# Kernel optimization log

Hardware: AMD Instinct MI355X
Metric: run time of the kernel (lower is better)

Reference implementation:

```python
import jax, jax.numpy as jnp
import numpy as np

B, S, D = 4, 2048, 1024
E, F, K = 8, 4096, 2  # num_experts, mlp_dim, experts_per_token


def setup_inputs() -> dict:
    key = jax.random.key(0)
    ks = jax.random.split(key, 5)
    scale_d = 1.0 / np.sqrt(D)
    scale_f = 1.0 / np.sqrt(F)
    return {
        "x": jax.random.normal(ks[0], (B, S, D), dtype=jnp.float32),
        "gate_w": jax.random.normal(ks[1], (D, E), dtype=jnp.float32) * scale_d,
        "wi0": jax.random.normal(ks[2], (E, D, F), dtype=jnp.float32) * scale_d,
        "wi1": jax.random.normal(ks[3], (E, D, F), dtype=jnp.float32) * scale_d,
        "wo": jax.random.normal(ks[4], (E, F, D), dtype=jnp.float32) * scale_f,
    }


def reference(x, gate_w, wi0, wi1, wo):
    # Gating: [B,S,E] logits -> top-k values/indices -> softmax over the k selected
    gate_logits = jnp.einsum("bsd,de->bse", x, gate_w)
    topk_w, topk_idx = jax.lax.top_k(gate_logits, K)  # [B,S,K]
    topk_w = jax.nn.softmax(topk_w, axis=-1)

    num_experts = wi0.shape[0]
    out = jnp.zeros_like(x)
    # Faithful to the naive MoE loop: every expert MLP runs over all tokens,
    # output masked/weighted by the token's gate weight for that expert.
    for e in range(num_experts):
        w_e = jnp.sum((topk_idx == e) * topk_w, axis=-1)  # [B,S]
        h = jax.nn.silu(jnp.einsum("bsd,df->bsf", x, wi0[e])) * jnp.einsum(
            "bsd,df->bsf", x, wi1[e]
        )  # gated SiLU MLP intermediate [B,S,F]
        out = out + w_e[..., None] * jnp.einsum("bsf,fd->bsd", h, wo[e])
    return out
```

## Files before the change

kernel.cpp:

```cpp
#include <hip/hip_runtime.h>
#include <math.h>

#define TOKENS 8192
#define DDIM 1024
#define FDIM 4096
#define NEXP 8
#define CAP 8192
#define BM 128
#define BN 128
#define BK 32

typedef __bf16 bf16x8 __attribute__((ext_vector_type(8)));
typedef float f32x4 __attribute__((ext_vector_type(4)));

__device__ __forceinline__ unsigned short f2bf(float f) {
  union { float f; unsigned int u; } v; v.f = f;
  unsigned int u = v.u;
  return (unsigned short)((u + 0x7FFFu + ((u >> 16) & 1u)) >> 16);
}
__device__ __forceinline__ float bf2f(unsigned short h) {
  union { unsigned int u; float f; } v; v.u = ((unsigned int)h) << 16;
  return v.f;
}

__device__ __forceinline__ void load_lds16(const void* g, void* l) {
  __builtin_amdgcn_global_load_lds(
      (const __attribute__((address_space(1))) void*)g,
      (__attribute__((address_space(3))) void*)l, 16, 0, 0);
}


__global__ void k_convert_x(const float* __restrict__ x, unsigned short* __restrict__ xb) {
  int i = (blockIdx.x * 256 + threadIdx.x) * 4;
  float4 v = *(const float4*)(x + i);
  ushort4 o;
  o.x = f2bf(v.x); o.y = f2bf(v.y); o.z = f2bf(v.z); o.w = f2bf(v.w);
  *(ushort4*)(xb + i) = o;
}

__global__ void k_tconv(const float* __restrict__ in, unsigned short* __restrict__ out,
                        int R, int C) {
  __shared__ float tile[32][132];
  size_t mat = (size_t)R * C;
  const float* src = in + (size_t)blockIdx.z * mat;
  unsigned short* dst = out + (size_t)blockIdx.z * mat;
  int c0 = blockIdx.x * 128, r0 = blockIdx.y * 32;
  int t = threadIdx.x;
#pragma unroll
  for (int i = 0; i < 4; ++i) {
    int idx = i * 1024 + t * 4;
    int r = idx >> 7, c = idx & 127;
    float4 v = *(const float4*)(src + (size_t)(r0 + r) * C + (c0 + c));
    *(float4*)&tile[r][c] = v;
  }
  __syncthreads();
#pragma unroll
  for (int i = 0; i < 4; ++i) {
    int idx = i * 1024 + t * 4;
    int c = idx >> 5, r = idx & 31;
    ushort4 o;
    o.x = f2bf(tile[r + 0][c]);
    o.y = f2bf(tile[r + 1][c]);
    o.z = f2bf(tile[r + 2][c]);
    o.w = f2bf(tile[r + 3][c]);
    *(ushort4*)(dst + (size_t)(c0 + c) * R + (r0 + r)) = o;
  }
}


__global__ void k_zero(int* __restrict__ counts) {
  if (threadIdx.x < NEXP) counts[threadIdx.x] = 0;
}

__global__ void k_gate(const float* __restrict__ x, const float* __restrict__ gw,
                       int* __restrict__ counts, int* __restrict__ tok_list,
                       float* __restrict__ wgt_list, int* __restrict__ tok_slot) {
  int wave = threadIdx.x >> 6, lane = threadIdx.x & 63;
  int t = blockIdx.x * 4 + wave;
  const float* xr = x + (size_t)t * DDIM;
  float acc[NEXP];
#pragma unroll
  for (int e = 0; e < NEXP; ++e) acc[e] = 0.f;
  for (int d = lane; d < DDIM; d += 64) {
    float xv = xr[d];
    const float* g = gw + d * NEXP;
#pragma unroll
    for (int e = 0; e < NEXP; ++e) acc[e] += xv * g[e];
  }
#pragma unroll
  for (int e = 0; e < NEXP; ++e) {
#pragma unroll
    for (int off = 32; off > 0; off >>= 1) acc[e] += __shfl_down(acc[e], off, 64);
  }
  if (lane == 0) {
    int e0 = 0; float v0 = acc[0];
#pragma unroll
    for (int e = 1; e < NEXP; ++e) if (acc[e] > v0) { v0 = acc[e]; e0 = e; }
    int e1 = -1; float v1 = -3.0e38f;
#pragma unroll
    for (int e = 0; e < NEXP; ++e) if (e != e0 && acc[e] > v1) { v1 = acc[e]; e1 = e; }
    float p1 = expf(v1 - v0);
    float s = 1.0f + p1;
    float w0 = 1.0f / s, w1 = p1 / s;
    int pos0 = atomicAdd(&counts[e0], 1);
    tok_list[e0 * CAP + pos0] = t;
    wgt_list[e0 * CAP + pos0] = w0;
    tok_slot[t * 2 + 0] = e0 * CAP + pos0;
    int pos1 = atomicAdd(&counts[e1], 1);
    tok_list[e1 * CAP + pos1] = t;
    wgt_list[e1 * CAP + pos1] = w1;
    tok_slot[t * 2 + 1] = e1 * CAP + pos1;
  }
}

__global__ void k_scan(const int* __restrict__ counts, int* __restrict__ bases) {
  if (threadIdx.x == 0) {
    int s = 0;
    for (int e = 0; e < NEXP; ++e) { bases[e] = s; s += counts[e]; }
  }
}


__global__ __launch_bounds__(256, 2) void k_gemm1(
    const unsigned short* __restrict__ xb, const unsigned short* __restrict__ w0t,
    const unsigned short* __restrict__ w1t, const int* __restrict__ counts,
    const int* __restrict__ bases, const int* __restrict__ tok_list,
    unsigned short* __restrict__ H) {
  int e = blockIdx.z, mt = blockIdx.y, nt = blockIdx.x;
  int cnt = counts[e];
  int m0 = mt * BM;
  if (m0 >= cnt) return;
  int mv = min(BM, cnt - m0);
  int gbase = bases[e] + m0;

  __shared__ __align__(16) unsigned short As[BM * BK];
  __shared__ __align__(16) unsigned short B0s[BN * BK];
  __shared__ __align__(16) unsigned short B1s[BN * BK];
  __shared__ int toks[BM];

  int t = threadIdx.x;
  if (t < BM) toks[t] = tok_list[e * CAP + m0 + min(t, mv - 1)];
  __syncthreads();

  int wid = t >> 6, lane = t & 63;
  int wm = (wid >> 1) * 64, wn = (wid & 1) * 64;
  int fr = lane & 15, fq = lane >> 4;
  int csl = fq ^ ((fr >> 1) & 3);

  int row0 = t >> 2,        row1 = (t + 256) >> 2;
  int fq0 = (t & 3) ^ ((row0 >> 1) & 3);
  int fq1 = ((t + 256) & 3) ^ ((row1 >> 1) & 3);

  f32x4 acc0[4][4], acc1[4][4];
#pragma unroll
  for (int mi = 0; mi < 4; ++mi)
#pragma unroll
    for (int ni = 0; ni < 4; ++ni)
#pragma unroll
      for (int r = 0; r < 4; ++r) { acc0[mi][ni][r] = 0.f; acc1[mi][ni][r] = 0.f; }

  const unsigned short* b0p = w0t + ((size_t)e * FDIM + nt * BN) * DDIM;
  const unsigned short* b1p = w1t + ((size_t)e * FDIM + nt * BN) * DDIM;
  const size_t arow0 = (size_t)toks[row0] * DDIM;
  const size_t arow1 = (size_t)toks[row1] * DDIM;

  for (int kt = 0; kt < DDIM; kt += BK) {
    load_lds16(xb + arow0 + kt + fq0 * 8, As + t * 8);
    load_lds16(xb + arow1 + kt + fq1 * 8, As + (t + 256) * 8);
    load_lds16(b0p + (size_t)row0 * DDIM + kt + fq0 * 8, B0s + t * 8);
    load_lds16(b0p + (size_t)row1 * DDIM + kt + fq1 * 8, B0s + (t + 256) * 8);
    load_lds16(b1p + (size_t)row0 * DDIM + kt + fq0 * 8, B1s + t * 8);
    load_lds16(b1p + (size_t)row1 * DDIM + kt + fq1 * 8, B1s + (t + 256) * 8);
    __syncthreads();
    bf16x8 a[4], b0[4], b1[4];
#pragma unroll
    for (int mi = 0; mi < 4; ++mi)
      a[mi] = *(const bf16x8*)(As + (wm + mi * 16 + fr) * BK + csl * 8);
#pragma unroll
    for (int ni = 0; ni < 4; ++ni) {
      b0[ni] = *(const bf16x8*)(B0s + (wn + ni * 16 + fr) * BK + csl * 8);
      b1[ni] = *(const bf16x8*)(B1s + (wn + ni * 16 + fr) * BK + csl * 8);
    }
#pragma unroll
    for (int mi = 0; mi < 4; ++mi)
#pragma unroll
      for (int ni = 0; ni < 4; ++ni) {
        acc0[mi][ni] = __builtin_amdgcn_mfma_f32_16x16x32_bf16(a[mi], b0[ni], acc0[mi][ni], 0, 0, 0);
        acc1[mi][ni] = __builtin_amdgcn_mfma_f32_16x16x32_bf16(a[mi], b1[ni], acc1[mi][ni], 0, 0, 0);
      }
    __syncthreads();
  }

  int n0 = nt * BN + wn;
#pragma unroll
  for (int mi = 0; mi < 4; ++mi) {
    int mloc = wm + mi * 16 + fq * 4;
#pragma unroll
    for (int ni = 0; ni < 4; ++ni) {
      int col = n0 + ni * 16 + fr;
#pragma unroll
      for (int r = 0; r < 4; ++r) {
        int mrow = mloc + r;
        if (mrow < mv) {
          float g = acc0[mi][ni][r];
          float hv = (g / (1.0f + expf(-g))) * acc1[mi][ni][r];
          H[(size_t)(gbase + mrow) * FDIM + col] = f2bf(hv);
        }
      }
    }
  }
}


__global__ __launch_bounds__(256, 2) void k_gemm2(
    const unsigned short* __restrict__ H, const unsigned short* __restrict__ wot,
    const int* __restrict__ counts, const int* __restrict__ bases,
    unsigned short* __restrict__ O) {
  int e = blockIdx.z, mt = blockIdx.y, nt = blockIdx.x;
  int cnt = counts[e];
  int m0 = mt * BM;
  if (m0 >= cnt) return;
  int mv = min(BM, cnt - m0);
  int gbase = bases[e] + m0;

  __shared__ __align__(16) unsigned short As[BM * BK];
  __shared__ __align__(16) unsigned short Bs[BN * BK];

  int t = threadIdx.x;
  int wid = t >> 6, lane = t & 63;
  int wm = (wid >> 1) * 64, wn = (wid & 1) * 64;
  int fr = lane & 15, fq = lane >> 4;
  int csl = fq ^ ((fr >> 1) & 3);

  int row0 = t >> 2,        row1 = (t + 256) >> 2;
  int fq0 = (t & 3) ^ ((row0 >> 1) & 3);
  int fq1 = ((t + 256) & 3) ^ ((row1 >> 1) & 3);

  f32x4 acc[4][4];
#pragma unroll
  for (int mi = 0; mi < 4; ++mi)
#pragma unroll
    for (int ni = 0; ni < 4; ++ni)
#pragma unroll
      for (int r = 0; r < 4; ++r) acc[mi][ni][r] = 0.f;

  const unsigned short* bp = wot + ((size_t)e * DDIM + nt * BN) * FDIM;
  const size_t arow0 = (size_t)(gbase + min(row0, mv - 1)) * FDIM;
  const size_t arow1 = (size_t)(gbase + min(row1, mv - 1)) * FDIM;

  for (int kt = 0; kt < FDIM; kt += BK) {
    load_lds16(H + arow0 + kt + fq0 * 8, As + t * 8);
    load_lds16(H + arow1 + kt + fq1 * 8, As + (t + 256) * 8);
    load_lds16(bp + (size_t)row0 * FDIM + kt + fq0 * 8, Bs + t * 8);
    load_lds16(bp + (size_t)row1 * FDIM + kt + fq1 * 8, Bs + (t + 256) * 8);
    __syncthreads();
    bf16x8 a[4], b[4];
#pragma unroll
    for (int mi = 0; mi < 4; ++mi)
      a[mi] = *(const bf16x8*)(As + (wm + mi * 16 + fr) * BK + csl * 8);
#pragma unroll
    for (int ni = 0; ni < 4; ++ni)
      b[ni] = *(const bf16x8*)(Bs + (wn + ni * 16 + fr) * BK + csl * 8);
#pragma unroll
    for (int mi = 0; mi < 4; ++mi)
#pragma unroll
      for (int ni = 0; ni < 4; ++ni)
        acc[mi][ni] = __builtin_amdgcn_mfma_f32_16x16x32_bf16(a[mi], b[ni], acc[mi][ni], 0, 0, 0);
    __syncthreads();
  }

  int n0 = nt * BN + wn;
#pragma unroll
  for (int mi = 0; mi < 4; ++mi) {
    int mloc = wm + mi * 16 + fq * 4;
#pragma unroll
    for (int ni = 0; ni < 4; ++ni) {
      int col = n0 + ni * 16 + fr;
#pragma unroll
      for (int r = 0; r < 4; ++r) {
        int mrow = mloc + r;
        if (mrow < mv)
          O[(size_t)(gbase + mrow) * DDIM + col] = f2bf(acc[mi][ni][r]);
      }
    }
  }
}


__global__ void k_combine(const unsigned short* __restrict__ O, const int* __restrict__ bases,
                          const int* __restrict__ tok_slot, const float* __restrict__ wgt_list,
                          float* __restrict__ out) {
  int t = blockIdx.x;
  int s0 = tok_slot[t * 2 + 0];
  int s1 = tok_slot[t * 2 + 1];
  int g0 = bases[s0 / CAP] + (s0 & (CAP - 1));
  int g1 = bases[s1 / CAP] + (s1 & (CAP - 1));
  float w0 = wgt_list[s0], w1 = wgt_list[s1];
  int d = threadIdx.x * 4;
  ushort4 a = *(const ushort4*)(O + (size_t)g0 * DDIM + d);
  ushort4 b = *(const ushort4*)(O + (size_t)g1 * DDIM + d);
  float4 r;
  r.x = w0 * bf2f(a.x) + w1 * bf2f(b.x);
  r.y = w0 * bf2f(a.y) + w1 * bf2f(b.y);
  r.z = w0 * bf2f(a.z) + w1 * bf2f(b.z);
  r.w = w0 * bf2f(a.w) + w1 * bf2f(b.w);
  *(float4*)(out + (size_t)t * DDIM + d) = r;
}


extern "C" void kernel_launch(void* const* d_in, const int* in_sizes, int n_in,
                              void* d_out, int out_size, void* d_ws, size_t ws_size,
                              hipStream_t stream) {
  const float* x   = (const float*)d_in[0];
  const float* gw  = (const float*)d_in[1];
  const float* wi0 = (const float*)d_in[2];
  const float* wi1 = (const float*)d_in[3];
  const float* wo  = (const float*)d_in[4];
  float* out = (float*)d_out;

  char* p = (char*)d_ws;
  unsigned short* xb  = (unsigned short*)p; p += (size_t)TOKENS * DDIM * 2;
  unsigned short* w0t = (unsigned short*)p; p += (size_t)NEXP * FDIM * DDIM * 2;
  unsigned short* w1t = (unsigned short*)p; p += (size_t)NEXP * FDIM * DDIM * 2;
  unsigned short* wot = (unsigned short*)p; p += (size_t)NEXP * DDIM * FDIM * 2;
  unsigned short* H   = (unsigned short*)p; p += (size_t)2 * TOKENS * FDIM * 2;
  unsigned short* O   = (unsigned short*)p; p += (size_t)2 * TOKENS * DDIM * 2;
  int*   counts   = (int*)p; p += 256;
  int*   bases    = (int*)p; p += 256;
  int*   tok_list = (int*)p; p += (size_t)NEXP * CAP * 4;
  float* wgt_list = (float*)p; p += (size_t)NEXP * CAP * 4;
  int*   tok_slot = (int*)p; p += (size_t)TOKENS * 2 * 4;

  k_convert_x<<<(TOKENS * DDIM) / 1024, 256, 0, stream>>>(x, xb);
  k_tconv<<<dim3(FDIM / 128, DDIM / 32, NEXP), 256, 0, stream>>>(wi0, w0t, DDIM, FDIM);
  k_tconv<<<dim3(FDIM / 128, DDIM / 32, NEXP), 256, 0, stream>>>(wi1, w1t, DDIM, FDIM);
  k_tconv<<<dim3(DDIM / 128, FDIM / 32, NEXP), 256, 0, stream>>>(wo, wot, FDIM, DDIM);

  k_zero<<<1, 64, 0, stream>>>(counts);
  k_gate<<<TOKENS / 4, 256, 0, stream>>>(x, gw, counts, tok_list, wgt_list, tok_slot);
  k_scan<<<1, 64, 0, stream>>>(counts, bases);

  k_gemm1<<<dim3(FDIM / BN, CAP / BM, NEXP), 256, 0, stream>>>(xb, w0t, w1t, counts, bases, tok_list, H);
  k_gemm2<<<dim3(DDIM / BN, CAP / BM, NEXP), 256, 0, stream>>>(H, wot, counts, bases, O);

  k_combine<<<TOKENS, 256, 0, stream>>>(O, bases, tok_slot, wgt_list, out);
}
```

Before: 1.267 ms.

## Double GEMM K-tile, remap blocks for XCD locality, fuse x conversion into gating

```diff
diff --git a/kernel.cpp b/kernel.cpp
--- a/kernel.cpp
+++ b/kernel.cpp
@@ -8,7 +8,7 @@
 #define CAP 8192
 #define BM 128
 #define BN 128
-#define BK 32
+#define BK 64
 
 typedef __bf16 bf16x8 __attribute__((ext_vector_type(8)));
 typedef float f32x4 __attribute__((ext_vector_type(4)));
@@ -27,15 +27,6 @@
   __builtin_amdgcn_global_load_lds(
       (const __attribute__((address_space(1))) void*)g,
       (__attribute__((address_space(3))) void*)l, 16, 0, 0);
-}
-
-
-__global__ void k_convert_x(const float* __restrict__ x, unsigned short* __restrict__ xb) {
-  int i = (blockIdx.x * 256 + threadIdx.x) * 4;
-  float4 v = *(const float4*)(x + i);
-  ushort4 o;
-  o.x = f2bf(v.x); o.y = f2bf(v.y); o.z = f2bf(v.z); o.w = f2bf(v.w);
-  *(ushort4*)(xb + i) = o;
 }
 
 __global__ void k_tconv(const float* __restrict__ in, unsigned short* __restrict__ out,
@@ -73,16 +64,19 @@
 }
 
 __global__ void k_gate(const float* __restrict__ x, const float* __restrict__ gw,
+                       unsigned short* __restrict__ xb,
                        int* __restrict__ counts, int* __restrict__ tok_list,
                        float* __restrict__ wgt_list, int* __restrict__ tok_slot) {
   int wave = threadIdx.x >> 6, lane = threadIdx.x & 63;
   int t = blockIdx.x * 4 + wave;
   const float* xr = x + (size_t)t * DDIM;
+  unsigned short* xbr = xb + (size_t)t * DDIM;
   float acc[NEXP];
 #pragma unroll
   for (int e = 0; e < NEXP; ++e) acc[e] = 0.f;
   for (int d = lane; d < DDIM; d += 64) {
     float xv = xr[d];
+    xbr[d] = f2bf(xv);
     const float* g = gw + d * NEXP;
 #pragma unroll
     for (int e = 0; e < NEXP; ++e) acc[e] += xv * g[e];
@@ -121,12 +115,20 @@
 }
 
 
+
 __global__ __launch_bounds__(256, 2) void k_gemm1(
     const unsigned short* __restrict__ xb, const unsigned short* __restrict__ w0t,
     const unsigned short* __restrict__ w1t, const int* __restrict__ counts,
     const int* __restrict__ bases, const int* __restrict__ tok_list,
     unsigned short* __restrict__ H) {
-  int e = blockIdx.z, mt = blockIdx.y, nt = blockIdx.x;
+  int b = blockIdx.x;
+  int xcd = b & 7, j = b >> 3;
+  int i8 = j & 7, grp = j >> 3;
+  int G = grp * 8 + xcd;
+  int e = G >> 8;
+  int mt = (G >> 2) & 63;
+  int nt = ((G & 3) << 3) | i8;
+
   int cnt = counts[e];
   int m0 = mt * BM;
   if (m0 >= cnt) return;
@@ -145,11 +147,20 @@
   int wid = t >> 6, lane = t & 63;
   int wm = (wid >> 1) * 64, wn = (wid & 1) * 64;
   int fr = lane & 15, fq = lane >> 4;
-  int csl = fq ^ ((fr >> 1) & 3);
-
-  int row0 = t >> 2,        row1 = (t + 256) >> 2;
-  int fq0 = (t & 3) ^ ((row0 >> 1) & 3);
-  int fq1 = ((t + 256) & 3) ^ ((row1 >> 1) & 3);
+  int sw = fr & 7;
+  int co0 = (fq ^ sw) * 8;
+  int co1 = ((4 | fq) ^ sw) * 8;
+
+  int srow[4], soff[4];
+#pragma unroll
+  for (int r = 0; r < 4; ++r) {
+    int s = t + r * 256;
+    srow[r] = s >> 3;
+    soff[r] = ((s & 7) ^ (srow[r] & 7)) * 8;
+  }
+  size_t arow[4];
+#pragma unroll
+  for (int r = 0; r < 4; ++r) arow[r] = (size_t)toks[srow[r]] * DDIM + soff[r];
 
   f32x4 acc0[4][4], acc1[4][4];
 #pragma unroll
@@ -161,33 +172,36 @@
 
   const unsigned short* b0p = w0t + ((size_t)e * FDIM + nt * BN) * DDIM;
   const unsigned short* b1p = w1t + ((size_t)e * FDIM + nt * BN) * DDIM;
-  const size_t arow0 = (size_t)toks[row0] * DDIM;
-  const size_t arow1 = (size_t)toks[row1] * DDIM;
 
   for (int kt = 0; kt < DDIM; kt += BK) {
-    load_lds16(xb + arow0 + kt + fq0 * 8, As + t * 8);
-    load_lds16(xb + arow1 + kt + fq1 * 8, As + (t + 256) * 8);
-    load_lds16(b0p + (size_t)row0 * DDIM + kt + fq0 * 8, B0s + t * 8);
-    load_lds16(b0p + (size_t)row1 * DDIM + kt + fq1 * 8, B0s + (t + 256) * 8);
-    load_lds16(b1p + (size_t)row0 * DDIM + kt + fq0 * 8, B1s + t * 8);
-    load_lds16(b1p + (size_t)row1 * DDIM + kt + fq1 * 8, B1s + (t + 256) * 8);
+#pragma unroll
+    for (int r = 0; r < 4; ++r) {
+      int s = t + r * 256;
+      load_lds16(xb + arow[r] + kt, As + s * 8);
+      load_lds16(b0p + (size_t)srow[r] * DDIM + soff[r] + kt, B0s + s * 8);
+      load_lds16(b1p + (size_t)srow[r] * DDIM + soff[r] + kt, B1s + s * 8);
+    }
     __syncthreads();
-    bf16x8 a[4], b0[4], b1[4];
-#pragma unroll
-    for (int mi = 0; mi < 4; ++mi)
-      a[mi] = *(const bf16x8*)(As + (wm + mi * 16 + fr) * BK + csl * 8);
-#pragma unroll
-    for (int ni = 0; ni < 4; ++ni) {
-      b0[ni] = *(const bf16x8*)(B0s + (wn + ni * 16 + fr) * BK + csl * 8);
-      b1[ni] = *(const bf16x8*)(B1s + (wn + ni * 16 + fr) * BK + csl * 8);
-    }
-#pragma unroll
-    for (int mi = 0; mi < 4; ++mi)
+#pragma unroll
+    for (int kh = 0; kh < 2; ++kh) {
+      int co = kh ? co1 : co0;
+      bf16x8 a[4], b0[4], b1[4];
+#pragma unroll
+      for (int mi = 0; mi < 4; ++mi)
+        a[mi] = *(const bf16x8*)(As + (wm + mi * 16 + fr) * BK + co);
 #pragma unroll
       for (int ni = 0; ni < 4; ++ni) {
-        acc0[mi][ni] = __builtin_amdgcn_mfma_f32_16x16x32_bf16(a[mi], b0[ni], acc0[mi][ni], 0, 0, 0);
-        acc1[mi][ni] = __builtin_amdgcn_mfma_f32_16x16x32_bf16(a[mi], b1[ni], acc1[mi][ni], 0, 0, 0);
+        b0[ni] = *(const bf16x8*)(B0s + (wn + ni * 16 + fr) * BK + co);
+        b1[ni] = *(const bf16x8*)(B1s + (wn + ni * 16 + fr) * BK + co);
       }
+#pragma unroll
+      for (int mi = 0; mi < 4; ++mi)
+#pragma unroll
+        for (int ni = 0; ni < 4; ++ni) {
+          acc0[mi][ni] = __builtin_amdgcn_mfma_f32_16x16x32_bf16(a[mi], b0[ni], acc0[mi][ni], 0, 0, 0);
+          acc1[mi][ni] = __builtin_amdgcn_mfma_f32_16x16x32_bf16(a[mi], b1[ni], acc1[mi][ni], 0, 0, 0);
+        }
+    }
     __syncthreads();
   }
 
@@ -216,7 +230,14 @@
     const unsigned short* __restrict__ H, const unsigned short* __restrict__ wot,
     const int* __restrict__ counts, const int* __restrict__ bases,
     unsigned short* __restrict__ O) {
-  int e = blockIdx.z, mt = blockIdx.y, nt = blockIdx.x;
+  int b = blockIdx.x;
+  int xcd = b & 7, j = b >> 3;
+  int i8 = j & 7, grp = j >> 3;
+  int G = grp * 8 + xcd;
+  int e = G >> 6;
+  int mt = G & 63;
+  int nt = i8;
+
   int cnt = counts[e];
   int m0 = mt * BM;
   if (m0 >= cnt) return;
@@ -230,11 +251,21 @@
   int wid = t >> 6, lane = t & 63;
   int wm = (wid >> 1) * 64, wn = (wid & 1) * 64;
   int fr = lane & 15, fq = lane >> 4;
-  int csl = fq ^ ((fr >> 1) & 3);
-
-  int row0 = t >> 2,        row1 = (t + 256) >> 2;
-  int fq0 = (t & 3) ^ ((row0 >> 1) & 3);
-  int fq1 = ((t + 256) & 3) ^ ((row1 >> 1) & 3);
+  int sw = fr & 7;
+  int co0 = (fq ^ sw) * 8;
+  int co1 = ((4 | fq) ^ sw) * 8;
+
+  int srow[4], soff[4];
+#pragma unroll
+  for (int r = 0; r < 4; ++r) {
+    int s = t + r * 256;
+    srow[r] = s >> 3;
+    soff[r] = ((s & 7) ^ (srow[r] & 7)) * 8;
+  }
+  size_t arow[4];
+#pragma unroll
+  for (int r = 0; r < 4; ++r)
+    arow[r] = (size_t)(gbase + min(srow[r], mv - 1)) * FDIM + soff[r];
 
   f32x4 acc[4][4];
 #pragma unroll
@@ -245,27 +276,31 @@
       for (int r = 0; r < 4; ++r) acc[mi][ni][r] = 0.f;
 
   const unsigned short* bp = wot + ((size_t)e * DDIM + nt * BN) * FDIM;
-  const size_t arow0 = (size_t)(gbase + min(row0, mv - 1)) * FDIM;
-  const size_t arow1 = (size_t)(gbase + min(row1, mv - 1)) * FDIM;
 
   for (int kt = 0; kt < FDIM; kt += BK) {
-    load_lds16(H + arow0 + kt + fq0 * 8, As + t * 8);
-    load_lds16(H + arow1 + kt + fq1 * 8, As + (t + 256) * 8);
-    load_lds16(bp + (size_t)row0 * FDIM + kt + fq0 * 8, Bs + t * 8);
-    load_lds16(bp + (size_t)row1 * FDIM + kt + fq1 * 8, Bs + (t + 256) * 8);
+#pragma unroll
+    for (int r = 0; r < 4; ++r) {
+      int s = t + r * 256;
+      load_lds16(H + arow[r] + kt, As + s * 8);
+      load_lds16(bp + (size_t)srow[r] * FDIM + soff[r] + kt, Bs + s * 8);
+    }
     __syncthreads();
-    bf16x8 a[4], b[4];
-#pragma unroll
-    for (int mi = 0; mi < 4; ++mi)
-      a[mi] = *(const bf16x8*)(As + (wm + mi * 16 + fr) * BK + csl * 8);
-#pragma unroll
-    for (int ni = 0; ni < 4; ++ni)
-      b[ni] = *(const bf16x8*)(Bs + (wn + ni * 16 + fr) * BK + csl * 8);
-#pragma unroll
-    for (int mi = 0; mi < 4; ++mi)
+#pragma unroll
+    for (int kh = 0; kh < 2; ++kh) {
+      int co = kh ? co1 : co0;
+      bf16x8 a[4], bb[4];
+#pragma unroll
+      for (int mi = 0; mi < 4; ++mi)
+        a[mi] = *(const bf16x8*)(As + (wm + mi * 16 + fr) * BK + co);
 #pragma unroll
       for (int ni = 0; ni < 4; ++ni)
-        acc[mi][ni] = __builtin_amdgcn_mfma_f32_16x16x32_bf16(a[mi], b[ni], acc[mi][ni], 0, 0, 0);
+        bb[ni] = *(const bf16x8*)(Bs + (wn + ni * 16 + fr) * BK + co);
+#pragma unroll
+      for (int mi = 0; mi < 4; ++mi)
+#pragma unroll
+        for (int ni = 0; ni < 4; ++ni)
+          acc[mi][ni] = __builtin_amdgcn_mfma_f32_16x16x32_bf16(a[mi], bb[ni], acc[mi][ni], 0, 0, 0);
+    }
     __syncthreads();
   }
 
@@ -331,17 +366,16 @@
   float* wgt_list = (float*)p; p += (size_t)NEXP * CAP * 4;
   int*   tok_slot = (int*)p; p += (size_t)TOKENS * 2 * 4;
 
-  k_convert_x<<<(TOKENS * DDIM) / 1024, 256, 0, stream>>>(x, xb);
   k_tconv<<<dim3(FDIM / 128, DDIM / 32, NEXP), 256, 0, stream>>>(wi0, w0t, DDIM, FDIM);
   k_tconv<<<dim3(FDIM / 128, DDIM / 32, NEXP), 256, 0, stream>>>(wi1, w1t, DDIM, FDIM);
   k_tconv<<<dim3(DDIM / 128, FDIM / 32, NEXP), 256, 0, stream>>>(wo, wot, FDIM, DDIM);
 
   k_zero<<<1, 64, 0, stream>>>(counts);
-  k_gate<<<TOKENS / 4, 256, 0, stream>>>(x, gw, counts, tok_list, wgt_list, tok_slot);
+  k_gate<<<TOKENS / 4, 256, 0, stream>>>(x, gw, xb, counts, tok_list, wgt_list, tok_slot);
   k_scan<<<1, 64, 0, stream>>>(counts, bases);
 
-  k_gemm1<<<dim3(FDIM / BN, CAP / BM, NEXP), 256, 0, stream>>>(xb, w0t, w1t, counts, bases, tok_list, H);
-  k_gemm2<<<dim3(DDIM / BN, CAP / BM, NEXP), 256, 0, stream>>>(H, wot, counts, bases, O);
+  k_gemm1<<<(FDIM / BN) * (CAP / BM) * NEXP, 256, 0, stream>>>(xb, w0t, w1t, counts, bases, tok_list, H);
+  k_gemm2<<<(DDIM / BN) * (CAP / BM) * NEXP, 256, 0, stream>>>(H, wot, counts, bases, O);
 
   k_combine<<<TOKENS, 256, 0, stream>>>(O, bases, tok_slot, wgt_list, out);
 }
```

After: 1.159 ms. -8.5%, faster.
